# Kernel optimization log

Measured on AMD Instinct MI355X. Metric: run time of the kernel, lower is better.

Reference implementation:

```python
import jax, jax.numpy as jnp
import numpy as np

N_DYADIC = 0  # dyadic refinement order 'n' from SigLoss_MMD.__init__


def _sig_gram(X, Y, n):
    """Gram matrix of signature kernels k(x_i, y_j) via the first-order
    finite-difference PDE scheme used by sig_kernels_f/fb_mmd:
        K[i+1,j+1] = K[i+1,j] + K[i,j+1] + K[i,j]*(<dx_i, dy_j> - 1)
    with dyadically refined increments dx = (x_{t+1}-x_t)/2^n repeated 2^n times.
    X: (A, M, D), Y: (B, N, D) -> returns (A, B) = K[:, :, -1, -1].
    The row recurrence is a cumulative sum, so each PDE row is one cumsum
    (fully vectorized over all (A,B) pairs); lax.scan runs over rows.
    """
    f = 2 ** n
    incX = jnp.repeat((X[:, 1:] - X[:, :-1]) / f, f, axis=1)  # (A, MM, D)
    incY = jnp.repeat((Y[:, 1:] - Y[:, :-1]) / f, f, axis=1)  # (B, NN, D)
    Mmat = jnp.einsum('aid,bjd->abij', incX, incY)            # (A, B, MM, NN)
    A, B, MM, NN = Mmat.shape
    ones_col = jnp.ones((A, B, 1), Mmat.dtype)
    row0 = jnp.ones((A, B, NN + 1), Mmat.dtype)               # K[0, :] = 1

    def step(prev_row, Mrow):  # prev_row: (A,B,NN+1), Mrow: (A,B,NN)
        # K[i+1,j+1] - K[i+1,j] = K[i,j+1] + K[i,j]*(M[i,j]-1)  -> cumsum
        inc = prev_row[..., 1:] + prev_row[..., :-1] * (Mrow - 1.0)
        new_row = jnp.concatenate([ones_col, 1.0 + jnp.cumsum(inc, axis=-1)], axis=-1)
        return new_row, None

    last_row, _ = jax.lax.scan(step, row0, jnp.moveaxis(Mmat, 2, 0))
    return last_row[..., -1]  # (A, B)


def setup_inputs() -> dict:
    key = jax.random.key(0)
    kx, ky = jax.random.split(key)
    A, M, D = 64, 128, 128
    SCALE = 0.025  # keeps increment inner products small so the PDE stays bounded
    X = SCALE * jax.random.normal(kx, (A, M, D), dtype=jnp.float32)
    Y = SCALE * jax.random.normal(ky, (A, M, D), dtype=jnp.float32)
    return {"X": X, "Y": Y}


def reference(X, Y):
    K_XX = _sig_gram(X, X, N_DYADIC)
    K_YY = _sig_gram(Y, Y, N_DYADIC)
    K_XY = _sig_gram(X, Y, N_DYADIC)
    mmd_squared = jnp.mean(K_XX) + jnp.mean(K_YY) - 2.0 * jnp.mean(K_XY)
    return mmd_squared
```

## Files before the change

kernel.cpp:

```cpp
#include <hip/hip_runtime.h>
#include <hip/hip_bf16.h>

#define MM 127
#define CHUNK_U16 4096
#define MAT_U16   16384
#define ARR_U16   1048576
#define QS_STRIDE 136
#define QS_DWORDS (64 * QS_STRIDE)

typedef __attribute__((ext_vector_type(8))) short short8;
typedef __attribute__((ext_vector_type(4))) float floatx4;

__device__ __forceinline__ unsigned short f2bf_rne(float x) {
  unsigned int u = __float_as_uint(x);
  u += 0x7FFFu + ((u >> 16) & 1u);
  return (unsigned short)(u >> 16);
}

__device__ __forceinline__ void gload_lds16(const void* g, void* l) {
  __builtin_amdgcn_global_load_lds(
      (const __attribute__((address_space(1))) unsigned int*)g,
      (__attribute__((address_space(3))) unsigned int*)l, 16, 0, 0);
}

__device__ __forceinline__ float wave_shr1(float x) {
  return __int_as_float(__builtin_amdgcn_update_dpp(
      0, __float_as_int(x), 0x138, 0xf, 0xf, true));
}

__global__ __launch_bounds__(256) void prep_kernel(
    const float* __restrict__ X, const float* __restrict__ Y,
    unsigned short* __restrict__ base, float* __restrict__ acc)
{
  if (blockIdx.x == 0 && threadIdx.x == 0) acc[0] = 0.f;
  const int bid = blockIdx.x;
  const int c = bid & 3;
  const int m = (bid >> 2) & 63;
  const int isY = bid >> 8;
  const float* src = (isY ? Y : X) + m * 128 * 128;
  unsigned short* dst = base + isY * ARR_U16 + m * MAT_U16 + c * CHUNK_U16;

  for (int s = threadIdx.x; s < 512; s += 256) {
    const int r = s >> 2;
    const int g = (s & 3) ^ (r & 3);
    uint4 hv = make_uint4(0, 0, 0, 0);
    if (r < MM) {
      const float* p = src + r * 128 + c * 32 + g * 8;
      float4 u0 = *reinterpret_cast<const float4*>(p);
      float4 u1 = *reinterpret_cast<const float4*>(p + 4);
      float4 v0 = *reinterpret_cast<const float4*>(p + 128);
      float4 v1 = *reinterpret_cast<const float4*>(p + 132);
      float d[8] = {v0.x - u0.x, v0.y - u0.y, v0.z - u0.z, v0.w - u0.w,
                    v1.x - u1.x, v1.y - u1.y, v1.z - u1.z, v1.w - u1.w};
      unsigned int hw[4];
#pragma unroll
      for (int e = 0; e < 4; ++e) {
        float2 rr; rr.x = d[2 * e]; rr.y = d[2 * e + 1];
        __hip_bfloat162 hp = __float22bfloat162_rn(rr);
        unsigned int hu; __builtin_memcpy(&hu, &hp, 4);
        hw[e] = hu;
      }
      hv = make_uint4(hw[0], hw[1], hw[2], hw[3]);
    }
    *reinterpret_cast<uint4*>(dst + s * 8) = hv;
  }
}

__global__ __launch_bounds__(256, 4) void sig_pair_kernel(
    const unsigned short* __restrict__ base, float* __restrict__ acc)
{
  __shared__ unsigned int smw[QS_DWORDS];
  unsigned short* const sm = reinterpret_cast<unsigned short*>(smw);
  const int tid = threadIdx.x;
  const int bid = blockIdx.x;

  float w;
  int a, b, srcA, srcB;
  if (bid < 4160) {
    int p = bid;
    srcA = 0;
    if (p >= 2080) { p -= 2080; srcA = 1; }
    srcB = srcA;
    int ia = (int)((sqrtf(8.0f * (float)p + 1.0f) - 1.0f) * 0.5f);
    while ((ia + 1) * (ia + 2) / 2 <= p) ia++;
    while (ia * (ia + 1) / 2 > p) ia--;
    int ib = p - ia * (ia + 1) / 2;
    a = ia; b = ib;
    w = (a == b ? 1.0f : 2.0f) / 4096.0f;
  } else {
    int p = bid - 4160;
    a = p >> 6; b = p & 63;
    srcA = 0; srcB = 1;
    w = -2.0f / 4096.0f;
  }
  const unsigned short* Am = base + srcA * ARR_U16 + a * MAT_U16;
  const unsigned short* Bm = base + srcB * ARR_U16 + b * MAT_U16;

  const int wid = tid >> 6, lane = tid & 63;
  const int row0 = (wid >> 1) * 64, col0 = (wid & 1) * 64;
  const int lrow = lane & 15, quad = lane >> 4;

  const unsigned short* gp = ((wid < 2) ? Am : Bm) + (wid & 1) * 2048 + lane * 8;
  const unsigned int dq = wid * 2048;

  floatx4 acc4[4][4];
#pragma unroll
  for (int tr = 0; tr < 4; ++tr)
#pragma unroll
    for (int tc = 0; tc < 4; ++tc) acc4[tr][tc] = (floatx4){0.f, 0.f, 0.f, 0.f};

#pragma unroll
  for (int s = 0; s < 4; ++s)
    gload_lds16(gp + s * 512, &sm[dq + s * 512]);

  for (int c = 0; c < 4; ++c) {
    __syncthreads();
    if (c < 3) {
      const unsigned short* g = gp + (c + 1) * CHUNK_U16;
      const unsigned int db_ = ((c + 1) & 1) * 8192 + dq;
#pragma unroll
      for (int s = 0; s < 4; ++s)
        gload_lds16(g + s * 512, &sm[db_ + s * 512]);
    }
    const unsigned int bb = (c & 1) * 8192;
    short8 bh[4];
#pragma unroll
    for (int tc = 0; tc < 4; ++tc) {
      int r = col0 + tc * 16 + lrow;
      int off = r * 32 + ((quad ^ (r & 3)) * 8);
      bh[tc] = *reinterpret_cast<const short8*>(&sm[bb + 4096 + off]);
    }
#pragma unroll
    for (int tr = 0; tr < 4; ++tr) {
      int r = row0 + tr * 16 + lrow;
      int off = r * 32 + ((quad ^ (r & 3)) * 8);
      short8 ah = *reinterpret_cast<const short8*>(&sm[bb + off]);
#pragma unroll
      for (int tc = 0; tc < 4; ++tc)
        acc4[tr][tc] = __builtin_amdgcn_mfma_f32_16x16x32_bf16(ah, bh[tc], acc4[tr][tc], 0, 0, 0);
    }
  }
  __syncthreads();

  for (int i = tid; i < QS_DWORDS; i += 256) smw[i] = 0u;
  __syncthreads();

#pragma unroll
  for (int tr = 0; tr < 4; ++tr) {
#pragma unroll
    for (int tc = 0; tc < 4; ++tc) {
      int jm = col0 + tc * 16 + lrow;
#pragma unroll
      for (int e = 0; e < 4; ++e) {
        int im = row0 + tr * 16 + quad * 4 + e;
        if (im < MM && jm < MM) {
          int lt = (jm + 1) >> 1;
          int phys = im + jm + 5 - 4 * (lt >> 1) - 4 * (lt & 1);
          int half = (jm & 1) ? 0 : 1;
          sm[(lt * QS_STRIDE + phys) * 2 + half] = f2bf_rne(acc4[tr][tc][e]);
        }
      }
    }
  }
  __syncthreads();

  if (wid == (bid & 3)) {
    const int l = lane;
    const int shift = 4 * (l >> 1) + 4 * (l & 1) - 4;
    const unsigned int lbase = l * QS_STRIDE;

    auto loadg = [&](int g) -> uint4 {
      int pb = 4 * g - shift;
      pb = pb < 0 ? 132 : (pb > 128 ? 128 : pb);
      return *reinterpret_cast<const uint4*>(&smw[lbase + pb]);
    };

    float curE = 1.f, curO = 1.f;
    float npE = (l == 0) ? 0.f : 1.f, npO = 1.f;
    uint4 P0 = loadg(0), P1 = loadg(1);

    for (int g = 0; g < 63; ++g) {
      const uint4 cur = P0;
      P0 = P1;
      if (g < 62) P1 = loadg(g + 2);
      unsigned int uu[4] = {cur.x, cur.y, cur.z, cur.w};
#pragma unroll
      for (int e = 0; e < 4; ++e) {
        unsigned int u = uu[e];
        float mE = __uint_as_float(u << 16) - 1.0f;
        float mO = __uint_as_float(u & 0xFFFF0000u) - 1.0f;
        float ncE = wave_shr1(curO);
        float ncO = curE;
        float vE = (curE + npE * mE) + ncE;
        float vO = (curO + npO * mO) + ncO;
        npE = ncE; npO = ncO;
        curE = vE; curO = vO;
      }
    }
    {
      unsigned int uu[2] = {P0.x, P0.y};
#pragma unroll
      for (int e = 0; e < 2; ++e) {
        unsigned int u = uu[e];
        float mE = __uint_as_float(u << 16) - 1.0f;
        float mO = __uint_as_float(u & 0xFFFF0000u) - 1.0f;
        float ncE = wave_shr1(curO);
        float ncO = curE;
        float vE = (curE + npE * mE) + ncE;
        float vO = (curO + npO * mO) + ncO;
        npE = ncE; npO = ncO;
        curE = vE; curO = vO;
      }
    }
    if (l == 63) atomicAdd(acc, w * curO);
  }
}

__global__ void finalize_kernel(const float* __restrict__ acc,
                                unsigned int* __restrict__ out) {
  float v = acc[0];
  __hip_bfloat16 bv = __float2bfloat16(v);
  unsigned short u;
  __builtin_memcpy(&u, &bv, sizeof(u));
  out[0] = ((unsigned int)u << 16) | (unsigned int)u;
}

extern "C" void kernel_launch(void* const* d_in, const int* in_sizes, int n_in,
                              void* d_out, int out_size, void* d_ws, size_t ws_size,
                              hipStream_t stream) {
  const float* X = (const float*)d_in[0];
  const float* Y = (const float*)d_in[1];
  float* acc = (float*)d_ws;
  unsigned short* base = (unsigned short*)((char*)d_ws + 1024);

  prep_kernel<<<512, 256, 0, stream>>>(X, Y, base, acc);
  sig_pair_kernel<<<8256, 256, 0, stream>>>(base, acc);
  finalize_kernel<<<1, 1, 0, stream>>>(acc, (unsigned int*)d_out);
}
```

Baseline: 201.6 us.

## Spread atomics over bins, fuse finalize via last-block counter, pack recurrence math

The single global atomic accumulator is replaced by 64 padded bins to reduce atomic contention. The separate finalize kernel is removed: a completion counter lets the last finishing block sum the bins and write the bf16 output, saving one launch. The prep kernel now launches twice as many blocks, with one element per thread, and the PDE recurrence uses packed two-wide float vectors with fma. The last-block pattern depends on threadfence ordering and changes the summation order of the result.

Result: slower. 302.9 us (+50.3%).

```diff
diff --git a/kernel.cpp b/kernel.cpp
--- a/kernel.cpp
+++ b/kernel.cpp
@@ -7,9 +7,11 @@
 #define ARR_U16   1048576
 #define QS_STRIDE 136
 #define QS_DWORDS (64 * QS_STRIDE)
+#define NBIN 64
 
 typedef __attribute__((ext_vector_type(8))) short short8;
 typedef __attribute__((ext_vector_type(4))) float floatx4;
+typedef __attribute__((ext_vector_type(2))) float f32x2;
 
 __device__ __forceinline__ unsigned short f2bf_rne(float x) {
   unsigned int u = __float_as_uint(x);
@@ -30,44 +32,49 @@
 
 __global__ __launch_bounds__(256) void prep_kernel(
     const float* __restrict__ X, const float* __restrict__ Y,
-    unsigned short* __restrict__ base, float* __restrict__ acc)
+    unsigned short* __restrict__ base, float* __restrict__ bins,
+    unsigned int* __restrict__ counter)
 {
-  if (blockIdx.x == 0 && threadIdx.x == 0) acc[0] = 0.f;
+  if (blockIdx.x == 0) {
+    if (threadIdx.x < NBIN) bins[threadIdx.x * 32] = 0.f;
+    if (threadIdx.x == 64) counter[0] = 0u;
+  }
   const int bid = blockIdx.x;
-  const int c = bid & 3;
-  const int m = (bid >> 2) & 63;
-  const int isY = bid >> 8;
+  const int isY = bid >> 9;
+  const int m = (bid >> 3) & 63;
+  const int c = (bid >> 1) & 3;
+  const int h = bid & 1;
   const float* src = (isY ? Y : X) + m * 128 * 128;
   unsigned short* dst = base + isY * ARR_U16 + m * MAT_U16 + c * CHUNK_U16;
 
-  for (int s = threadIdx.x; s < 512; s += 256) {
-    const int r = s >> 2;
-    const int g = (s & 3) ^ (r & 3);
-    uint4 hv = make_uint4(0, 0, 0, 0);
-    if (r < MM) {
-      const float* p = src + r * 128 + c * 32 + g * 8;
-      float4 u0 = *reinterpret_cast<const float4*>(p);
-      float4 u1 = *reinterpret_cast<const float4*>(p + 4);
-      float4 v0 = *reinterpret_cast<const float4*>(p + 128);
-      float4 v1 = *reinterpret_cast<const float4*>(p + 132);
-      float d[8] = {v0.x - u0.x, v0.y - u0.y, v0.z - u0.z, v0.w - u0.w,
-                    v1.x - u1.x, v1.y - u1.y, v1.z - u1.z, v1.w - u1.w};
-      unsigned int hw[4];
-#pragma unroll
-      for (int e = 0; e < 4; ++e) {
-        float2 rr; rr.x = d[2 * e]; rr.y = d[2 * e + 1];
-        __hip_bfloat162 hp = __float22bfloat162_rn(rr);
-        unsigned int hu; __builtin_memcpy(&hu, &hp, 4);
-        hw[e] = hu;
-      }
-      hv = make_uint4(hw[0], hw[1], hw[2], hw[3]);
-    }
-    *reinterpret_cast<uint4*>(dst + s * 8) = hv;
-  }
+  const int s = h * 256 + threadIdx.x;
+  const int r = s >> 2;
+  const int g = (s & 3) ^ (r & 3);
+  uint4 hv = make_uint4(0, 0, 0, 0);
+  if (r < MM) {
+    const float* p = src + r * 128 + c * 32 + g * 8;
+    float4 u0 = *reinterpret_cast<const float4*>(p);
+    float4 u1 = *reinterpret_cast<const float4*>(p + 4);
+    float4 v0 = *reinterpret_cast<const float4*>(p + 128);
+    float4 v1 = *reinterpret_cast<const float4*>(p + 132);
+    float d[8] = {v0.x - u0.x, v0.y - u0.y, v0.z - u0.z, v0.w - u0.w,
+                  v1.x - u1.x, v1.y - u1.y, v1.z - u1.z, v1.w - u1.w};
+    unsigned int hw[4];
+#pragma unroll
+    for (int e = 0; e < 4; ++e) {
+      float2 rr; rr.x = d[2 * e]; rr.y = d[2 * e + 1];
+      __hip_bfloat162 hp = __float22bfloat162_rn(rr);
+      unsigned int hu; __builtin_memcpy(&hu, &hp, 4);
+      hw[e] = hu;
+    }
+    hv = make_uint4(hw[0], hw[1], hw[2], hw[3]);
+  }
+  *reinterpret_cast<uint4*>(dst + s * 8) = hv;
 }
 
 __global__ __launch_bounds__(256, 4) void sig_pair_kernel(
-    const unsigned short* __restrict__ base, float* __restrict__ acc)
+    const unsigned short* __restrict__ base, float* __restrict__ bins,
+    unsigned int* __restrict__ counter, unsigned int* __restrict__ out)
 {
   __shared__ unsigned int smw[QS_DWORDS];
   unsigned short* const sm = reinterpret_cast<unsigned short*>(smw);
@@ -175,26 +182,28 @@
       return *reinterpret_cast<const uint4*>(&smw[lbase + pb]);
     };
 
-    float curE = 1.f, curO = 1.f;
-    float npE = (l == 0) ? 0.f : 1.f, npO = 1.f;
+    f32x2 cur; cur.x = 1.f; cur.y = 1.f;
+    f32x2 np;  np.x = (l == 0) ? 0.f : 1.f; np.y = 1.f;
+    const f32x2 mone = {-1.f, -1.f};
     uint4 P0 = loadg(0), P1 = loadg(1);
 
     for (int g = 0; g < 63; ++g) {
-      const uint4 cur = P0;
+      const uint4 curg = P0;
       P0 = P1;
       if (g < 62) P1 = loadg(g + 2);
-      unsigned int uu[4] = {cur.x, cur.y, cur.z, cur.w};
+      unsigned int uu[4] = {curg.x, curg.y, curg.z, curg.w};
 #pragma unroll
       for (int e = 0; e < 4; ++e) {
         unsigned int u = uu[e];
-        float mE = __uint_as_float(u << 16) - 1.0f;
-        float mO = __uint_as_float(u & 0xFFFF0000u) - 1.0f;
-        float ncE = wave_shr1(curO);
-        float ncO = curE;
-        float vE = (curE + npE * mE) + ncE;
-        float vO = (curO + npO * mO) + ncO;
-        npE = ncE; npO = ncO;
-        curE = vE; curO = vO;
+        f32x2 m1;
+        m1.x = __uint_as_float(u << 16);
+        m1.y = __uint_as_float(u & 0xFFFF0000u);
+        m1 = m1 + mone;
+        f32x2 nc;
+        nc.x = wave_shr1(cur.y);
+        nc.y = cur.x;
+        cur = __builtin_elementwise_fma(np, m1, cur) + nc;
+        np = nc;
       }
     }
     {
@@ -202,27 +211,32 @@
 #pragma unroll
       for (int e = 0; e < 2; ++e) {
         unsigned int u = uu[e];
-        float mE = __uint_as_float(u << 16) - 1.0f;
-        float mO = __uint_as_float(u & 0xFFFF0000u) - 1.0f;
-        float ncE = wave_shr1(curO);
-        float ncO = curE;
-        float vE = (curE + npE * mE) + ncE;
-        float vO = (curO + npO * mO) + ncO;
-        npE = ncE; npO = ncO;
-        curE = vE; curO = vO;
-      }
-    }
-    if (l == 63) atomicAdd(acc, w * curO);
-  }
-}
-
-__global__ void finalize_kernel(const float* __restrict__ acc,
-                                unsigned int* __restrict__ out) {
-  float v = acc[0];
-  __hip_bfloat16 bv = __float2bfloat16(v);
-  unsigned short u;
-  __builtin_memcpy(&u, &bv, sizeof(u));
-  out[0] = ((unsigned int)u << 16) | (unsigned int)u;
+        f32x2 m1;
+        m1.x = __uint_as_float(u << 16);
+        m1.y = __uint_as_float(u & 0xFFFF0000u);
+        m1 = m1 + mone;
+        f32x2 nc;
+        nc.x = wave_shr1(cur.y);
+        nc.y = cur.x;
+        cur = __builtin_elementwise_fma(np, m1, cur) + nc;
+        np = nc;
+      }
+    }
+    if (l == 63) {
+      atomicAdd(&bins[(bid & 63) * 32], w * cur.y);
+      __threadfence();
+      unsigned int t = atomicAdd(counter, 1u);
+      if (t == 8255u) {
+        __threadfence();
+        float v = 0.f;
+        for (int i = 0; i < NBIN; ++i) v += atomicAdd(&bins[i * 32], 0.f);
+        __hip_bfloat16 bv = __float2bfloat16(v);
+        unsigned short us;
+        __builtin_memcpy(&us, &bv, sizeof(us));
+        out[0] = ((unsigned int)us << 16) | (unsigned int)us;
+      }
+    }
+  }
 }
 
 extern "C" void kernel_launch(void* const* d_in, const int* in_sizes, int n_in,
@@ -230,10 +244,11 @@
                               hipStream_t stream) {
   const float* X = (const float*)d_in[0];
   const float* Y = (const float*)d_in[1];
-  float* acc = (float*)d_ws;
-  unsigned short* base = (unsigned short*)((char*)d_ws + 1024);
-
-  prep_kernel<<<512, 256, 0, stream>>>(X, Y, base, acc);
-  sig_pair_kernel<<<8256, 256, 0, stream>>>(base, acc);
-  finalize_kernel<<<1, 1, 0, stream>>>(acc, (unsigned int*)d_out);
-}
+  float* bins = (float*)d_ws;
+  unsigned int* counter = (unsigned int*)((char*)d_ws + 8192);
+  unsigned short* base = (unsigned short*)((char*)d_ws + 16384);
+
+  prep_kernel<<<1024, 256, 0, stream>>>(X, Y, base, bins, counter);
+  sig_pair_kernel<<<8256, 256, 0, stream>>>(base, bins, counter,
+                                            (unsigned int*)d_out);
+}
```
